# Kernel optimization log

Measured on AMD Instinct MI355X. Metric: run time of the kernel, lower is better.

Reference implementation:

```python
import jax, jax.numpy as jnp
import numpy as np

N = 10000        # nodes
E = 160000       # edges (before self-loops)
NFEAT = 256
NHID = 128
H = 4            # heads
NCLASS = 40
NLAYERS = 2
DT = 1.0
ALPHA = 1.0
GAMMA = 1.0
NEG_SLOPE = 0.2  # GATConv leaky_relu slope


def setup_inputs() -> dict:
    key = jax.random.key(0)
    ks = jax.random.split(key, 12)

    def glorot(k, shape):
        fan_in, fan_out = shape[-1], shape[0]
        lim = (6.0 / (fan_in + fan_out)) ** 0.5
        return jax.random.uniform(k, shape, jnp.float32, -lim, lim)

    return {
        "x": jax.random.normal(ks[0], (N, NFEAT), jnp.float32),
        "edge_index": jax.random.randint(ks[1], (2, E), 0, N, jnp.int64),
        "enc_w": glorot(ks[2], (NHID, NFEAT)),
        "enc_b": jnp.zeros((NHID,), jnp.float32),
        "res_w": glorot(ks[3], (H * NHID, NHID)),
        "res_b": jnp.zeros((H * NHID,), jnp.float32),
        "gat_w": glorot(ks[4], (H * NHID, NHID)),
        "att_src": glorot(ks[5], (H, NHID)) * 0.1,
        "att_dst": glorot(ks[6], (H, NHID)) * 0.1,
        "gat_b": jnp.zeros((H * NHID,), jnp.float32),
        "dec_w": glorot(ks[7], (NCLASS, NHID)),
        "dec_b": jnp.zeros((NCLASS,), jnp.float32),
    }


def _gat_conv(x, src, dst, gat_w, att_src, att_dst, gat_b):
    # x: [N, NHID] -> per-head features [N, H, C]
    xh = (x @ gat_w.T).reshape(N, H, NHID)
    a_src = jnp.sum(xh * att_src[None], axis=-1)  # [N, H]
    a_dst = jnp.sum(xh * att_dst[None], axis=-1)  # [N, H]
    e = jax.nn.leaky_relu(a_src[src] + a_dst[dst], NEG_SLOPE)  # [E', H]
    # segment softmax over incoming edges of each destination node
    m = jax.ops.segment_max(e, dst, num_segments=N)            # [N, H]
    e = jnp.exp(e - m[dst])
    s = jax.ops.segment_sum(e, dst, num_segments=N)            # [N, H]
    alpha = e / s[dst]                                          # [E', H]
    msg = xh[src] * alpha[:, :, None]                           # [E', H, C]
    out = jax.ops.segment_sum(msg, dst, num_segments=N)         # [N, H, C]
    return out.reshape(N, H * NHID) + gat_b


def reference(x, edge_index, enc_w, enc_b, res_w, res_b, gat_w,
              att_src, att_dst, gat_b, dec_w, dec_b):
    # add self-loops (GATConv default)
    loop = jnp.arange(N, dtype=edge_index.dtype)
    src = jnp.concatenate([edge_index[0], loop])
    dst = jnp.concatenate([edge_index[1], loop])

    Y = jax.nn.relu(x @ enc_w.T + enc_b)  # [N, NHID]
    X = Y
    for _ in range(NLAYERS):
        conv = _gat_conv(X, src, dst, gat_w, att_src, att_dst, gat_b)  # [N, H*NHID]
        res = X @ res_w.T + res_b                                       # [N, H*NHID]
        # faithful to .view(n_nodes, -1, nheads).mean(-1): [N, NHID, H] -> mean over heads axis
        z = jax.nn.elu(conv + res).reshape(N, NHID, H).mean(axis=-1)    # [N, NHID]
        Y = Y + DT * (z - ALPHA * Y - GAMMA * X)
        X = X + DT * Y
    return X @ dec_w.T + dec_b  # [N, NCLASS]
```

## Files before the change

kernel.cpp:

```cpp
#include <hip/hip_runtime.h>
#include <math.h>

#define NN 10000
#define EE 160000
#define EP 170000
#define NFEAT 256
#define NHID 128
#define NH 4
#define HF 512
#define NCLASS 40
#define FCOLS 1088

typedef __attribute__((ext_vector_type(8))) short bf8;
typedef __attribute__((ext_vector_type(8))) unsigned short u16x8;
typedef __attribute__((ext_vector_type(4))) float f4;

__device__ __forceinline__ float leaky02(float x) { return x >= 0.0f ? x : 0.2f * x; }

__device__ __forceinline__ unsigned short f2bf(float f) {
    unsigned u = __builtin_bit_cast(unsigned, f);
    unsigned r = (u + 0x7FFF + ((u >> 16) & 1)) >> 16;
    return (unsigned short)r;
}
__device__ __forceinline__ float bf2f(unsigned short h) {
    return __builtin_bit_cast(float, (unsigned)h << 16);
}

__device__ __forceinline__ int swz(int row, int c) {
    return ((((c >> 3) ^ (row & 7)) << 3) | (c & 7));
}

__device__ __forceinline__ void gl_lds16(const unsigned short* g, unsigned short* l)
{
    __builtin_amdgcn_global_load_lds(
        (const __attribute__((address_space(1))) unsigned int*)g,
        (__attribute__((address_space(3))) unsigned int*)l, 16, 0, 0);
}

#define C_X   2560000
#define C_EW  (C_X + 32768)
#define C_FW  (C_EW + 131072)
#define C_DW  (C_FW + 5120)
#define CVT_B  1333
#define ATTW_B (CVT_B + 8)
#define TOT_B  (ATTW_B + 166)

__global__ __launch_bounds__(256)
void fused0_k(const float* __restrict__ x, const float* __restrict__ enc_w,
              const float* __restrict__ gat_w, const float* __restrict__ res_w,
              const float* __restrict__ dec_w,
              const float* __restrict__ att_src, const float* __restrict__ att_dst,
              const float* __restrict__ res_b, const float* __restrict__ gat_b,
              const int* __restrict__ ei,
              unsigned short* __restrict__ xhi, unsigned short* __restrict__ ewhi,
              unsigned short* __restrict__ fwhi, unsigned short* __restrict__ dwhi,
              float* __restrict__ biasRG, int* __restrict__ cnt)
{
    int bId = blockIdx.x;
    int t = threadIdx.x;
    if (bId < CVT_B) {
        int iu = bId * 256 + t;
        int i = iu * 8;
        if (i >= C_DW) return;
        const float* src = nullptr; unsigned short* ph; int j, row, c, Kd;
        if (i < C_X)       { j = i;        src = x;     ph = xhi;
                             row = j >> 8; c = j & 255; Kd = 256; }
        else if (i < C_EW) { j = i - C_X;  src = enc_w; ph = ewhi;
                             row = j >> 8; c = j & 255; Kd = 256; }
        else if (i < C_FW) { j = i - C_EW; ph = fwhi;
                             row = j >> 7; c = j & 127; Kd = 128; }
        else               { j = i - C_FW; src = dec_w; ph = dwhi;
                             row = j >> 7; c = j & 127; Kd = 128; }
        float4 v0, v1;
        if (src) { v0 = *(const float4*)(src + j); v1 = *(const float4*)(src + j + 4); }
        else {
            const float* s2 = (j < 65536) ? (gat_w + j) : (res_w + j - 65536);
            v0 = *(const float4*)s2; v1 = *(const float4*)(s2 + 4);
        }
        float vv[8] = {v0.x, v0.y, v0.z, v0.w, v1.x, v1.y, v1.z, v1.w};
        unsigned short hs[8];
#pragma unroll
        for (int k = 0; k < 8; ++k) hs[k] = f2bf(vv[k]);
        int outp = row * Kd + swz(row, c);
        *(u16x8*)(ph + outp) = *(u16x8*)hs;
    } else if (bId < ATTW_B) {
        __shared__ float sm[256];
        int b = bId - CVT_B;
        int is_dst = b >> 2, h = b & 3;
        const float* att = is_dst ? att_dst : att_src;
        int k = t & 127, half = t >> 7;
        float s = 0.0f;
#pragma unroll 4
        for (int c = half * 64; c < half * 64 + 64; ++c)
            s = fmaf(gat_w[(size_t)(h * 128 + c) * 128 + k], att[h * 128 + c], s);
        sm[t] = s;
        __syncthreads();
        if (t < 128) {
            float v = sm[t] + sm[t + 128];
            int R = 1024 + is_dst * 4 + h;
            fwhi[(size_t)R * 128 + swz(R, k)] = f2bf(v);
        }
        for (int i = b * 896 + t; i < (b + 1) * 896; i += 256)
            fwhi[1032 * 128 + i] = 0;
        if (b < 2) {
            int c = b * 256 + t;
            biasRG[c] = res_b[c] + gat_b[c];
        }
    } else {
        for (int e = (bId - ATTW_B) * 256 + t; e < EP; e += (TOT_B - ATTW_B) * 256) {
            int d = (e < EE) ? ei[EE + e] : (e - EE);
            atomicAdd(&cnt[d], 1);
        }
    }
}

template<int MODE, int KTILES, int MERGE>
__global__ __launch_bounds__(256)
void gemm3_k(const unsigned short* __restrict__ A, const unsigned short* __restrict__ B,
             const float* __restrict__ bias, float* __restrict__ outF,
             unsigned short* __restrict__ outH, unsigned short* __restrict__ outL,
             float* __restrict__ a_src, float* __restrict__ a_dst, int M,
             const int* __restrict__ ei, const int* __restrict__ cnt,
             int* __restrict__ row_ptr, int* __restrict__ cursor, int* __restrict__ csr)
{
    constexpr int K = KTILES * 128;
    __shared__ __align__(16) unsigned short smem[2 * 64 * 128];
    const int tid = threadIdx.x;

    if (MERGE && blockIdx.y == gridDim.y - 1) {
        if (MERGE == 1) {
            if (blockIdx.x != 0) return;
            int* smi = (int*)smem;
            int i0 = tid * 40, i1 = min(i0 + 40, NN);
            int part = 0;
            for (int i = i0; i < i1; ++i) part += cnt[i];
            smi[tid] = part;
            __syncthreads();
            for (int off = 1; off < 256; off <<= 1) {
                int v = (tid >= off) ? smi[tid - off] : 0;
                __syncthreads();
                smi[tid] += v;
                __syncthreads();
            }
            int run = smi[tid] - part;
            for (int i = i0; i < i1; ++i) { row_ptr[i] = run; run += cnt[i]; }
            if (tid == 255) row_ptr[NN] = run;
        } else {
            int stride = gridDim.x * 256;
            for (int e = blockIdx.x * 256 + tid; e < EP; e += stride) {
                int s, d;
                if (e < EE) { s = ei[e]; d = ei[EE + e]; } else { s = e - EE; d = s; }
                int pos = row_ptr[d] + atomicAdd(&cursor[d], 1);
                csr[pos] = s;
            }
        }
        return;
    }

    unsigned short* sA = smem;
    unsigned short* sB = smem + 8192;

    const int lane = tid & 63, wv = tid >> 6;
    const int wr = (wv >> 1) * 32, wc = (wv & 1) * 32;
    const int bm = blockIdx.x * 64, bn = blockIdx.y * 64;
    const int r16 = lane & 15, q4 = lane >> 4;

    f4 acc[2][2];
#pragma unroll
    for (int i = 0; i < 2; ++i)
#pragma unroll
        for (int j = 0; j < 2; ++j) acc[i][j] = (f4){0.f, 0.f, 0.f, 0.f};

    const int ra0 = wr + r16;
    const int rb0 = wc + r16;

    for (int kt = 0; kt < KTILES; ++kt) {
        if (kt) __syncthreads();
#pragma unroll
        for (int j = 0; j < 4; ++j) {
            int i = tid + j * 256;
            int row = i >> 4, u = i & 15;
            int arow = min(bm + row, M - 1);
            size_t ga = (size_t)arow * K + kt * 128 + u * 8;
            size_t gb = (size_t)(bn + row) * K + kt * 128 + u * 8;
            int lb = (wv * 64 + j * 256) * 8;
            gl_lds16(A + ga, sA + lb);
            gl_lds16(B + gb, sB + lb);
        }
        __syncthreads();

#pragma unroll
        for (int ks = 0; ks < 4; ++ks) {
            int u = ks * 4 + q4;
            int oa0 = ra0 * 128 + ((u ^ (ra0 & 7)) * 8);
            int ob0 = rb0 * 128 + ((u ^ (rb0 & 7)) * 8);
            int oa1 = oa0 + 16 * 128;
            int ob1 = ob0 + 16 * 128;
            bf8 A0 = *(const bf8*)(sA + oa0);
            bf8 A1 = *(const bf8*)(sA + oa1);
            bf8 B0 = *(const bf8*)(sB + ob0);
            bf8 B1 = *(const bf8*)(sB + ob1);

            acc[0][0] = __builtin_amdgcn_mfma_f32_16x16x32_bf16(A0, B0, acc[0][0], 0, 0, 0);
            acc[0][1] = __builtin_amdgcn_mfma_f32_16x16x32_bf16(A0, B1, acc[0][1], 0, 0, 0);
            acc[1][0] = __builtin_amdgcn_mfma_f32_16x16x32_bf16(A1, B0, acc[1][0], 0, 0, 0);
            acc[1][1] = __builtin_amdgcn_mfma_f32_16x16x32_bf16(A1, B1, acc[1][1], 0, 0, 0);
        }
    }

    const int rbase = q4 * 4;

    if (MODE == 0 || (MODE == 2 && bn >= 1024)) {
#pragma unroll
        for (int i = 0; i < 2; ++i)
#pragma unroll
            for (int j = 0; j < 2; ++j)
#pragma unroll
                for (int r = 0; r < 4; ++r) {
                    int row = bm + wr + i * 16 + rbase + r;
                    int col = bn + wc + j * 16 + r16;
                    if (row >= M) continue;
                    float v = acc[i][j][r];
                    if (MODE == 0) {
                        if (col < NCLASS)
                            outF[(size_t)row * NCLASS + col] = v + bias[col];
                    } else {
                        if (col < 1032) {
                            int h = col - 1024;
                            if (h < 4) a_src[row * 4 + h] = v;
                            else       a_dst[row * 4 + h - 4] = v;
                        }
                    }
                }
        return;
    }

    __syncthreads();
    float* sC = (float*)smem;
#pragma unroll
    for (int i = 0; i < 2; ++i)
#pragma unroll
        for (int j = 0; j < 2; ++j)
#pragma unroll
            for (int r = 0; r < 4; ++r)
                sC[(wr + i * 16 + rbase + r) * 65 + (wc + j * 16 + r16)] = acc[i][j][r];
    __syncthreads();

    int row = tid >> 2, seg = tid & 3, c0 = seg * 16;
    int grow = bm + row;
    if (grow < M) {
        float v[16];
#pragma unroll
        for (int k = 0; k < 16; ++k) v[k] = sC[row * 65 + c0 + k];

        if (MODE == 1) {
            unsigned short hs[16];
#pragma unroll
            for (int k = 0; k < 16; ++k)
                hs[k] = f2bf(fmaxf(v[k] + bias[bn + c0 + k], 0.0f));
#pragma unroll
            for (int uu = 0; uu < 2; ++uu) {
                int ug = (bn + c0) / 8 + uu;
                int pu = ug ^ (grow & 7);
                *(u16x8*)(outH + (size_t)grow * 128 + pu * 8) = *(u16x8*)(hs + uu * 8);
            }
        } else {
            if (bn < 512) {
                unsigned short hs[16];
#pragma unroll
                for (int k = 0; k < 16; ++k) hs[k] = f2bf(v[k]);
                *(u16x8*)(outH + (size_t)grow * 512 + bn + c0)     = *(u16x8*)hs;
                *(u16x8*)(outH + (size_t)grow * 512 + bn + c0 + 8) = *(u16x8*)(hs + 8);
            } else {
                unsigned short hs[16];
#pragma unroll
                for (int k = 0; k < 16; ++k) hs[k] = f2bf(v[k] + bias[bn - 512 + c0 + k]);
                *(u16x8*)(outL + (size_t)grow * 512 + (bn - 512) + c0)     = *(u16x8*)hs;
                *(u16x8*)(outL + (size_t)grow * 512 + (bn - 512) + c0 + 8) = *(u16x8*)(hs + 8);
            }
        }
    }
}

__global__ __launch_bounds__(256)
void agg_k(const int* __restrict__ row_ptr, const int* __restrict__ csr,
           const float* __restrict__ a_src, const float* __restrict__ a_dst,
           const unsigned short* __restrict__ xh_b, const unsigned short* __restrict__ resb,
           unsigned short* __restrict__ Xhi)
{
    int bx = blockIdx.x;
    int h  = bx / 2500;
    int ng = bx - h * 2500;
    int wv = threadIdx.x >> 6, lane = threadIdx.x & 63;
    int d = ng * 4 + wv;
    int beg = row_ptr[d], end = row_ptr[d + 1];
    int eg = lane >> 4, c16 = lane & 15;
    int cb = h * 128 + c16 * 8;
    float ad = a_dst[d * 4 + h];
    u16x8 rv = *(const u16x8*)(resb + (size_t)d * HF + cb);

    float acc[8];
#pragma unroll
    for (int k = 0; k < 8; ++k) acc[k] = 0.0f;
    float ssum = 0.0f;

    int e = beg;
    for (; e + 16 <= end; e += 16) {
        int sv[4]; float w[4]; u16x8 v[4];
#pragma unroll
        for (int q = 0; q < 4; ++q) sv[q] = csr[e + q * 4 + eg];
#pragma unroll
        for (int q = 0; q < 4; ++q) v[q] = *(const u16x8*)(xh_b + (size_t)sv[q] * HF + cb);
#pragma unroll
        for (int q = 0; q < 4; ++q) {
            w[q] = __expf(leaky02(a_src[sv[q] * 4 + h] + ad));
            ssum += w[q];
        }
#pragma unroll
        for (int q = 0; q < 4; ++q)
#pragma unroll
            for (int k = 0; k < 8; ++k) acc[k] = fmaf(w[q], bf2f(v[q][k]), acc[k]);
    }
    for (; e + 4 <= end; e += 4) {
        int s = csr[e + eg];
        u16x8 v = *(const u16x8*)(xh_b + (size_t)s * HF + cb);
        float w = __expf(leaky02(a_src[s * 4 + h] + ad));
        ssum += w;
#pragma unroll
        for (int k = 0; k < 8; ++k) acc[k] = fmaf(w, bf2f(v[k]), acc[k]);
    }
    if (e + eg < end) {
        int s = csr[e + eg];
        u16x8 v = *(const u16x8*)(xh_b + (size_t)s * HF + cb);
        float w = __expf(leaky02(a_src[s * 4 + h] + ad));
        ssum += w;
#pragma unroll
        for (int k = 0; k < 8; ++k) acc[k] = fmaf(w, bf2f(v[k]), acc[k]);
    }

#pragma unroll
    for (int off = 16; off <= 32; off <<= 1) {
        ssum += __shfl_xor(ssum, off);
#pragma unroll
        for (int k = 0; k < 8; ++k) acc[k] += __shfl_xor(acc[k], off);
    }

    float inv = 1.0f / ssum;
    float uv[8];
#pragma unroll
    for (int k = 0; k < 8; ++k) {
        float v = fmaf(acc[k], inv, bf2f(rv[k]));
        uv[k] = (v > 0.0f) ? v : expm1f(v);
    }
    float z0 = (uv[0] + uv[1] + uv[2] + uv[3]) * 0.25f;
    float z1 = (uv[4] + uv[5] + uv[6] + uv[7]) * 0.25f;
    if (eg == 0) {
        int col = h * 32 + c16 * 2;
        unsigned short h0b = f2bf(z0), h1b = f2bf(z1);
        size_t idx = (size_t)d * NHID + swz(d, col);
        *(unsigned*)(Xhi + idx) = ((unsigned)h1b << 16) | h0b;
    }
}

extern "C" void kernel_launch(void* const* d_in, const int* in_sizes, int n_in,
                              void* d_out, int out_size, void* d_ws, size_t ws_size,
                              hipStream_t stream)
{
    const float* x       = (const float*)d_in[0];
    const int*   ei      = (const int*)d_in[1];
    const float* enc_w   = (const float*)d_in[2];
    const float* enc_b   = (const float*)d_in[3];
    const float* res_w   = (const float*)d_in[4];
    const float* res_b   = (const float*)d_in[5];
    const float* gat_w   = (const float*)d_in[6];
    const float* att_src = (const float*)d_in[7];
    const float* att_dst = (const float*)d_in[8];
    const float* gat_b   = (const float*)d_in[9];
    const float* dec_w   = (const float*)d_in[10];
    const float* dec_b   = (const float*)d_in[11];
    float* out = (float*)d_out;

    char* p = (char*)d_ws;
    auto alloc = [&](size_t bytes) -> void* {
        void* r = (void*)p;
        p += (bytes + 255) & ~(size_t)255;
        return r;
    };
    float* a_src  = (float*)alloc(40000 * 4);
    float* a_dst  = (float*)alloc(40000 * 4);
    float* biasRG = (float*)alloc(512 * 4);
    unsigned short* xh_b = (unsigned short*)alloc(5120000 * 2);
    unsigned short* resb = (unsigned short*)alloc(5120000 * 2);
    unsigned short* Xhi  = (unsigned short*)alloc(1280000 * 2);
    unsigned short* xhi  = (unsigned short*)alloc(2560000 * 2);
    unsigned short* ewhi = (unsigned short*)alloc(32768 * 2);
    unsigned short* fwhi = (unsigned short*)alloc(FCOLS * 128 * 2);
    int* row_ptr = (int*)alloc(10004 * 4);
    int* csr     = (int*)alloc(170000 * 4);
    char* zbase = p;
    unsigned short* dwhi = (unsigned short*)alloc(8192 * 2);
    int* cnt    = (int*)alloc(10000 * 4);
    int* cursor = (int*)alloc(10000 * 4);
    size_t zbytes = (size_t)(p - zbase);

    hipMemsetAsync(zbase, 0, zbytes, stream);

    fused0_k<<<TOT_B, 256, 0, stream>>>(
        x, enc_w, gat_w, res_w, dec_w, att_src, att_dst, res_b, gat_b, ei,
        xhi, ewhi, fwhi, dwhi, biasRG, cnt);

    gemm3_k<1, 2, 1><<<dim3(157, 3), 256, 0, stream>>>(
        xhi, ewhi, enc_b, nullptr, Xhi, nullptr, nullptr, nullptr, NN,
        nullptr, cnt, row_ptr, nullptr, nullptr);

    gemm3_k<2, 1, 2><<<dim3(157, 18), 256, 0, stream>>>(
        Xhi, fwhi, biasRG, nullptr, xh_b, resb, a_src, a_dst, NN,
        ei, nullptr, row_ptr, cursor, csr);
    agg_k<<<10000, 256, 0, stream>>>(row_ptr, csr, a_src, a_dst, xh_b, resb, Xhi);

    gemm3_k<2, 1, 0><<<dim3(157, 17), 256, 0, stream>>>(
        Xhi, fwhi, biasRG, nullptr, xh_b, resb, a_src, a_dst, NN,
        nullptr, nullptr, nullptr, nullptr, nullptr);
    agg_k<<<10000, 256, 0, stream>>>(row_ptr, csr, a_src, a_dst, xh_b, resb, Xhi);

    gemm3_k<0, 1, 0><<<dim3(157, 1), 256, 0, stream>>>(
        Xhi, dwhi, dec_b, out, nullptr, nullptr, nullptr, nullptr, NN,
        nullptr, nullptr, nullptr, nullptr, nullptr);
}
```

Measured before the change: 206.8 us.

## Merge all stages into one persistent cooperative kernel with grid syncs

```diff
diff --git a/kernel.cpp b/kernel.cpp
--- a/kernel.cpp
+++ b/kernel.cpp
@@ -1,5 +1,8 @@
 #include <hip/hip_runtime.h>
+#include <hip/hip_cooperative_groups.h>
 #include <math.h>
+
+namespace cg = cooperative_groups;
 
 #define NN 10000
 #define EE 160000
@@ -9,7 +12,6 @@
 #define NH 4
 #define HF 512
 #define NCLASS 40
-#define FCOLS 1088
 
 typedef __attribute__((ext_vector_type(8))) short bf8;
 typedef __attribute__((ext_vector_type(8))) unsigned short u16x8;
@@ -41,129 +43,27 @@
 #define C_EW  (C_X + 32768)
 #define C_FW  (C_EW + 131072)
 #define C_DW  (C_FW + 5120)
-#define CVT_B  1333
-#define ATTW_B (CVT_B + 8)
-#define TOT_B  (ATTW_B + 166)
-
-__global__ __launch_bounds__(256)
-void fused0_k(const float* __restrict__ x, const float* __restrict__ enc_w,
-              const float* __restrict__ gat_w, const float* __restrict__ res_w,
-              const float* __restrict__ dec_w,
-              const float* __restrict__ att_src, const float* __restrict__ att_dst,
-              const float* __restrict__ res_b, const float* __restrict__ gat_b,
-              const int* __restrict__ ei,
-              unsigned short* __restrict__ xhi, unsigned short* __restrict__ ewhi,
-              unsigned short* __restrict__ fwhi, unsigned short* __restrict__ dwhi,
-              float* __restrict__ biasRG, int* __restrict__ cnt)
-{
-    int bId = blockIdx.x;
-    int t = threadIdx.x;
-    if (bId < CVT_B) {
-        int iu = bId * 256 + t;
-        int i = iu * 8;
-        if (i >= C_DW) return;
-        const float* src = nullptr; unsigned short* ph; int j, row, c, Kd;
-        if (i < C_X)       { j = i;        src = x;     ph = xhi;
-                             row = j >> 8; c = j & 255; Kd = 256; }
-        else if (i < C_EW) { j = i - C_X;  src = enc_w; ph = ewhi;
-                             row = j >> 8; c = j & 255; Kd = 256; }
-        else if (i < C_FW) { j = i - C_EW; ph = fwhi;
-                             row = j >> 7; c = j & 127; Kd = 128; }
-        else               { j = i - C_FW; src = dec_w; ph = dwhi;
-                             row = j >> 7; c = j & 127; Kd = 128; }
-        float4 v0, v1;
-        if (src) { v0 = *(const float4*)(src + j); v1 = *(const float4*)(src + j + 4); }
-        else {
-            const float* s2 = (j < 65536) ? (gat_w + j) : (res_w + j - 65536);
-            v0 = *(const float4*)s2; v1 = *(const float4*)(s2 + 4);
-        }
-        float vv[8] = {v0.x, v0.y, v0.z, v0.w, v1.x, v1.y, v1.z, v1.w};
-        unsigned short hs[8];
-#pragma unroll
-        for (int k = 0; k < 8; ++k) hs[k] = f2bf(vv[k]);
-        int outp = row * Kd + swz(row, c);
-        *(u16x8*)(ph + outp) = *(u16x8*)hs;
-    } else if (bId < ATTW_B) {
-        __shared__ float sm[256];
-        int b = bId - CVT_B;
-        int is_dst = b >> 2, h = b & 3;
-        const float* att = is_dst ? att_dst : att_src;
-        int k = t & 127, half = t >> 7;
-        float s = 0.0f;
-#pragma unroll 4
-        for (int c = half * 64; c < half * 64 + 64; ++c)
-            s = fmaf(gat_w[(size_t)(h * 128 + c) * 128 + k], att[h * 128 + c], s);
-        sm[t] = s;
-        __syncthreads();
-        if (t < 128) {
-            float v = sm[t] + sm[t + 128];
-            int R = 1024 + is_dst * 4 + h;
-            fwhi[(size_t)R * 128 + swz(R, k)] = f2bf(v);
-        }
-        for (int i = b * 896 + t; i < (b + 1) * 896; i += 256)
-            fwhi[1032 * 128 + i] = 0;
-        if (b < 2) {
-            int c = b * 256 + t;
-            biasRG[c] = res_b[c] + gat_b[c];
-        }
-    } else {
-        for (int e = (bId - ATTW_B) * 256 + t; e < EP; e += (TOT_B - ATTW_B) * 256) {
-            int d = (e < EE) ? ei[EE + e] : (e - EE);
-            atomicAdd(&cnt[d], 1);
-        }
-    }
-}
-
-template<int MODE, int KTILES, int MERGE>
-__global__ __launch_bounds__(256)
-void gemm3_k(const unsigned short* __restrict__ A, const unsigned short* __restrict__ B,
-             const float* __restrict__ bias, float* __restrict__ outF,
-             unsigned short* __restrict__ outH, unsigned short* __restrict__ outL,
-             float* __restrict__ a_src, float* __restrict__ a_dst, int M,
-             const int* __restrict__ ei, const int* __restrict__ cnt,
-             int* __restrict__ row_ptr, int* __restrict__ cursor, int* __restrict__ csr)
+#define CVT_U (C_DW / 8)
+
+template<int MODE, int KTILES>
+__device__ void gemm_job(int bx, int by,
+    const unsigned short* __restrict__ A, const unsigned short* __restrict__ B,
+    const float* __restrict__ bias, float* __restrict__ outF,
+    unsigned short* __restrict__ outH, unsigned short* __restrict__ outL,
+    float* __restrict__ a_srcW, float* __restrict__ a_dstW, int M,
+    unsigned short* smem)
 {
     constexpr int K = KTILES * 128;
-    __shared__ __align__(16) unsigned short smem[2 * 64 * 128];
     const int tid = threadIdx.x;
-
-    if (MERGE && blockIdx.y == gridDim.y - 1) {
-        if (MERGE == 1) {
-            if (blockIdx.x != 0) return;
-            int* smi = (int*)smem;
-            int i0 = tid * 40, i1 = min(i0 + 40, NN);
-            int part = 0;
-            for (int i = i0; i < i1; ++i) part += cnt[i];
-            smi[tid] = part;
-            __syncthreads();
-            for (int off = 1; off < 256; off <<= 1) {
-                int v = (tid >= off) ? smi[tid - off] : 0;
-                __syncthreads();
-                smi[tid] += v;
-                __syncthreads();
-            }
-            int run = smi[tid] - part;
-            for (int i = i0; i < i1; ++i) { row_ptr[i] = run; run += cnt[i]; }
-            if (tid == 255) row_ptr[NN] = run;
-        } else {
-            int stride = gridDim.x * 256;
-            for (int e = blockIdx.x * 256 + tid; e < EP; e += stride) {
-                int s, d;
-                if (e < EE) { s = ei[e]; d = ei[EE + e]; } else { s = e - EE; d = s; }
-                int pos = row_ptr[d] + atomicAdd(&cursor[d], 1);
-                csr[pos] = s;
-            }
-        }
-        return;
-    }
-
     unsigned short* sA = smem;
     unsigned short* sB = smem + 8192;
 
     const int lane = tid & 63, wv = tid >> 6;
     const int wr = (wv >> 1) * 32, wc = (wv & 1) * 32;
-    const int bm = blockIdx.x * 64, bn = blockIdx.y * 64;
+    const int bm = bx * 64, bn = by * 64;
     const int r16 = lane & 15, q4 = lane >> 4;
+
+    __syncthreads();
 
     f4 acc[2][2];
 #pragma unroll
@@ -227,8 +127,8 @@
                     } else {
                         if (col < 1032) {
                             int h = col - 1024;
-                            if (h < 4) a_src[row * 4 + h] = v;
-                            else       a_dst[row * 4 + h - 4] = v;
+                            if (h < 4) a_srcW[row * 4 + h] = v;
+                            else       a_dstW[row * 4 + h - 4] = v;
                         }
                     }
                 }
@@ -282,13 +182,12 @@
     }
 }
 
-__global__ __launch_bounds__(256)
-void agg_k(const int* __restrict__ row_ptr, const int* __restrict__ csr,
-           const float* __restrict__ a_src, const float* __restrict__ a_dst,
-           const unsigned short* __restrict__ xh_b, const unsigned short* __restrict__ resb,
-           unsigned short* __restrict__ Xhi)
+__device__ void agg_job(int bx,
+    const int* __restrict__ row_ptr, const int* __restrict__ csr,
+    const float* __restrict__ a_src, const float* __restrict__ a_dst,
+    const unsigned short* __restrict__ xh_b, const unsigned short* __restrict__ resb,
+    unsigned short* __restrict__ Xhi)
 {
-    int bx = blockIdx.x;
     int h  = bx / 2500;
     int ng = bx - h * 2500;
     int wv = threadIdx.x >> 6, lane = threadIdx.x & 63;
@@ -362,23 +261,181 @@
     }
 }
 
+struct MegaArgs {
+    const float *x, *enc_w, *enc_b, *res_b, *gat_w, *att_src, *att_dst, *gat_b, *dec_w, *dec_b;
+    const float *res_w;
+    const int* ei;
+    float* out;
+    float *a_src, *a_dst, *biasRG;
+    unsigned short *xh_b, *resb, *Xhi, *xhi, *ewhi, *fwhi, *dwhi;
+    int *row_ptr, *csr, *cnt, *cursor;
+};
+
+__global__ __launch_bounds__(256, 3)
+void mega_k(MegaArgs a)
+{
+    __shared__ __align__(16) unsigned short smem[2 * 64 * 128];
+    cg::grid_group gg = cg::this_grid();
+    const int g   = (int)gridDim.x;
+    const int bid = (int)blockIdx.x, tid = (int)threadIdx.x;
+    const int gtid = bid * 256 + tid;
+    const int gth  = g * 256;
+
+    {
+        int* dz = (int*)(a.dwhi + 40 * 128);
+        for (int i = gtid; i < 1536; i += gth) dz[i] = 0;
+        for (int i = gtid; i < NN; i += gth) { a.cnt[i] = 0; a.cursor[i] = 0; }
+    }
+    for (int iu = gtid; iu < CVT_U; iu += gth) {
+        int i = iu * 8;
+        const float* src = nullptr; unsigned short* ph; int j, row, c, Kd;
+        if (i < C_X)       { j = i;        src = a.x;     ph = a.xhi;
+                             row = j >> 8; c = j & 255; Kd = 256; }
+        else if (i < C_EW) { j = i - C_X;  src = a.enc_w; ph = a.ewhi;
+                             row = j >> 8; c = j & 255; Kd = 256; }
+        else if (i < C_FW) { j = i - C_EW; ph = a.fwhi;
+                             row = j >> 7; c = j & 127; Kd = 128; }
+        else               { j = i - C_FW; src = a.dec_w; ph = a.dwhi;
+                             row = j >> 7; c = j & 127; Kd = 128; }
+        float4 v0, v1;
+        if (src) { v0 = *(const float4*)(src + j); v1 = *(const float4*)(src + j + 4); }
+        else {
+            const float* s2 = (j < 65536) ? (a.gat_w + j) : (a.res_w + j - 65536);
+            v0 = *(const float4*)s2; v1 = *(const float4*)(s2 + 4);
+        }
+        float vv[8] = {v0.x, v0.y, v0.z, v0.w, v1.x, v1.y, v1.z, v1.w};
+        unsigned short hs[8];
+#pragma unroll
+        for (int k = 0; k < 8; ++k) hs[k] = f2bf(vv[k]);
+        int outp = row * Kd + swz(row, c);
+        *(u16x8*)(ph + outp) = *(u16x8*)hs;
+    }
+    if (bid < 8) {
+        float* sm = (float*)smem;
+        int b = bid, is_dst = b >> 2, h = b & 3;
+        const float* att = is_dst ? a.att_dst : a.att_src;
+        int k = tid & 127, half = tid >> 7;
+        float s = 0.0f;
+#pragma unroll 4
+        for (int c = half * 64; c < half * 64 + 64; ++c)
+            s = fmaf(a.gat_w[(size_t)(h * 128 + c) * 128 + k], att[h * 128 + c], s);
+        sm[tid] = s;
+        __syncthreads();
+        if (tid < 128) {
+            float v = sm[tid] + sm[tid + 128];
+            int R = 1024 + is_dst * 4 + h;
+            a.fwhi[(size_t)R * 128 + swz(R, k)] = f2bf(v);
+        }
+        for (int i = b * 896 + tid; i < (b + 1) * 896; i += 256)
+            a.fwhi[1032 * 128 + i] = 0;
+    }
+    if (bid == 8) {
+        a.biasRG[tid]       = a.res_b[tid]       + a.gat_b[tid];
+        a.biasRG[tid + 256] = a.res_b[tid + 256] + a.gat_b[tid + 256];
+    }
+    gg.sync();
+
+    {
+        int gb1 = min(314, g - 128);
+        if (bid < gb1) {
+            for (int j = bid; j < 314; j += gb1)
+                gemm_job<1, 2>(j % 157, j / 157, a.xhi, a.ewhi, a.enc_b,
+                               nullptr, a.Xhi, nullptr, nullptr, nullptr, NN, smem);
+        } else {
+            for (int e = (bid - gb1) * 256 + tid; e < EP; e += (g - gb1) * 256) {
+                int d = (e < EE) ? a.ei[EE + e] : (e - EE);
+                atomicAdd(&a.cnt[d], 1);
+            }
+        }
+    }
+    gg.sync();
+
+    {
+        int gb2 = g - 1;
+        if (bid < gb2) {
+            int cpb = (2669 + gb2 - 1) / gb2;
+            int j0 = bid * cpb, j1 = min(j0 + cpb, 2669);
+            for (int j = j0; j < j1; ++j)
+                gemm_job<2, 1>(j % 157, j / 157, a.Xhi, a.fwhi, a.biasRG,
+                               nullptr, a.xh_b, a.resb, a.a_src, a.a_dst, NN, smem);
+        } else {
+            int* smi = (int*)smem;
+            int i0 = tid * 40, i1 = min(i0 + 40, NN);
+            int part = 0;
+            for (int i = i0; i < i1; ++i) part += a.cnt[i];
+            smi[tid] = part;
+            __syncthreads();
+            for (int off = 1; off < 256; off <<= 1) {
+                int v = (tid >= off) ? smi[tid - off] : 0;
+                __syncthreads();
+                smi[tid] += v;
+                __syncthreads();
+            }
+            int run = smi[tid] - part;
+            for (int i = i0; i < i1; ++i) { a.row_ptr[i] = run; run += a.cnt[i]; }
+            if (tid == 255) a.row_ptr[NN] = run;
+        }
+    }
+    gg.sync();
+
+    for (int e = gtid; e < EP; e += gth) {
+        int s, d;
+        if (e < EE) { s = a.ei[e]; d = a.ei[EE + e]; } else { s = e - EE; d = s; }
+        int pos = a.row_ptr[d] + atomicAdd(&a.cursor[d], 1);
+        a.csr[pos] = s;
+    }
+    gg.sync();
+
+    {
+        int cpb = (NN + g - 1) / g;
+        int j0 = bid * cpb, j1 = min(j0 + cpb, NN);
+        for (int j = j0; j < j1; ++j)
+            agg_job(j, a.row_ptr, a.csr, a.a_src, a.a_dst, a.xh_b, a.resb, a.Xhi);
+    }
+    gg.sync();
+
+    {
+        int cpb = (2669 + g - 1) / g;
+        int j0 = bid * cpb, j1 = min(j0 + cpb, 2669);
+        for (int j = j0; j < j1; ++j)
+            gemm_job<2, 1>(j % 157, j / 157, a.Xhi, a.fwhi, a.biasRG,
+                           nullptr, a.xh_b, a.resb, a.a_src, a.a_dst, NN, smem);
+    }
+    gg.sync();
+
+    {
+        int cpb = (NN + g - 1) / g;
+        int j0 = bid * cpb, j1 = min(j0 + cpb, NN);
+        for (int j = j0; j < j1; ++j)
+            agg_job(j, a.row_ptr, a.csr, a.a_src, a.a_dst, a.xh_b, a.resb, a.Xhi);
+    }
+    gg.sync();
+
+    if (bid < 157)
+        gemm_job<0, 1>(bid, 0, a.Xhi, a.dwhi, a.dec_b, a.out,
+                       nullptr, nullptr, nullptr, nullptr, NN, smem);
+}
+
 extern "C" void kernel_launch(void* const* d_in, const int* in_sizes, int n_in,
                               void* d_out, int out_size, void* d_ws, size_t ws_size,
                               hipStream_t stream)
 {
-    const float* x       = (const float*)d_in[0];
-    const int*   ei      = (const int*)d_in[1];
-    const float* enc_w   = (const float*)d_in[2];
-    const float* enc_b   = (const float*)d_in[3];
-    const float* res_w   = (const float*)d_in[4];
-    const float* res_b   = (const float*)d_in[5];
-    const float* gat_w   = (const float*)d_in[6];
-    const float* att_src = (const float*)d_in[7];
-    const float* att_dst = (const float*)d_in[8];
-    const float* gat_b   = (const float*)d_in[9];
-    const float* dec_w   = (const float*)d_in[10];
-    const float* dec_b   = (const float*)d_in[11];
-    float* out = (float*)d_out;
+    (void)in_sizes; (void)n_in; (void)out_size; (void)ws_size;
+
+    MegaArgs a;
+    a.x       = (const float*)d_in[0];
+    a.ei      = (const int*)d_in[1];
+    a.enc_w   = (const float*)d_in[2];
+    a.enc_b   = (const float*)d_in[3];
+    a.res_w   = (const float*)d_in[4];
+    a.res_b   = (const float*)d_in[5];
+    a.gat_w   = (const float*)d_in[6];
+    a.att_src = (const float*)d_in[7];
+    a.att_dst = (const float*)d_in[8];
+    a.gat_b   = (const float*)d_in[9];
+    a.dec_w   = (const float*)d_in[10];
+    a.dec_b   = (const float*)d_in[11];
+    a.out     = (float*)d_out;
 
     char* p = (char*)d_ws;
     auto alloc = [&](size_t bytes) -> void* {
@@ -386,44 +443,38 @@
         p += (bytes + 255) & ~(size_t)255;
         return r;
     };
-    float* a_src  = (float*)alloc(40000 * 4);
-    float* a_dst  = (float*)alloc(40000 * 4);
-    float* biasRG = (float*)alloc(512 * 4);
-    unsigned short* xh_b = (unsigned short*)alloc(5120000 * 2);
-    unsigned short* resb = (unsigned short*)alloc(5120000 * 2);
-    unsigned short* Xhi  = (unsigned short*)alloc(1280000 * 2);
-    unsigned short* xhi  = (unsigned short*)alloc(2560000 * 2);
-    unsigned short* ewhi = (unsigned short*)alloc(32768 * 2);
-    unsigned short* fwhi = (unsigned short*)alloc(FCOLS * 128 * 2);
-    int* row_ptr = (int*)alloc(10004 * 4);
-    int* csr     = (int*)alloc(170000 * 4);
-    char* zbase = p;
-    unsigned short* dwhi = (unsigned short*)alloc(8192 * 2);
-    int* cnt    = (int*)alloc(10000 * 4);
-    int* cursor = (int*)alloc(10000 * 4);
-    size_t zbytes = (size_t)(p - zbase);
-
-    hipMemsetAsync(zbase, 0, zbytes, stream);
-
-    fused0_k<<<TOT_B, 256, 0, stream>>>(
-        x, enc_w, gat_w, res_w, dec_w, att_src, att_dst, res_b, gat_b, ei,
-        xhi, ewhi, fwhi, dwhi, biasRG, cnt);
-
-    gemm3_k<1, 2, 1><<<dim3(157, 3), 256, 0, stream>>>(
-        xhi, ewhi, enc_b, nullptr, Xhi, nullptr, nullptr, nullptr, NN,
-        nullptr, cnt, row_ptr, nullptr, nullptr);
-
-    gemm3_k<2, 1, 2><<<dim3(157, 18), 256, 0, stream>>>(
-        Xhi, fwhi, biasRG, nullptr, xh_b, resb, a_src, a_dst, NN,
-        ei, nullptr, row_ptr, cursor, csr);
-    agg_k<<<10000, 256, 0, stream>>>(row_ptr, csr, a_src, a_dst, xh_b, resb, Xhi);
-
-    gemm3_k<2, 1, 0><<<dim3(157, 17), 256, 0, stream>>>(
-        Xhi, fwhi, biasRG, nullptr, xh_b, resb, a_src, a_dst, NN,
-        nullptr, nullptr, nullptr, nullptr, nullptr);
-    agg_k<<<10000, 256, 0, stream>>>(row_ptr, csr, a_src, a_dst, xh_b, resb, Xhi);
-
-    gemm3_k<0, 1, 0><<<dim3(157, 1), 256, 0, stream>>>(
-        Xhi, dwhi, dec_b, out, nullptr, nullptr, nullptr, nullptr, NN,
-        nullptr, nullptr, nullptr, nullptr, nullptr);
-}
+    a.a_src   = (float*)alloc(40000 * 4);
+    a.a_dst   = (float*)alloc(40000 * 4);
+    a.biasRG  = (float*)alloc(512 * 4);
+    a.xh_b    = (unsigned short*)alloc(5120000 * 2);
+    a.resb    = (unsigned short*)alloc(5120000 * 2);
+    a.Xhi     = (unsigned short*)alloc(1280000 * 2);
+    a.xhi     = (unsigned short*)alloc(2560000 * 2);
+    a.ewhi    = (unsigned short*)alloc(32768 * 2);
+    a.fwhi    = (unsigned short*)alloc(1088 * 128 * 2);
+    a.row_ptr = (int*)alloc(10004 * 4);
+    a.csr     = (int*)alloc(170000 * 4);
+    a.dwhi    = (unsigned short*)alloc(8192 * 2);
+    a.cnt     = (int*)alloc(10000 * 4);
+    a.cursor  = (int*)alloc(10000 * 4);
+
+    static int s_mb = 0;
+    if (s_mb == 0) {
+        int mb = 0;
+        if (hipOccupancyMaxActiveBlocksPerMultiprocessor(
+                &mb, (const void*)mega_k, 256, 0) != hipSuccess || mb < 1)
+            mb = 3;
+        if (mb > 5) mb = 5;
+        if (mb < 2) mb = 2;
+        s_mb = mb;
+    }
+    void* kargs[] = { (void*)&a };
+    for (int t = 0; t < 3; ++t) {
+        hipError_t err = hipLaunchCooperativeKernel(
+            (const void*)mega_k, dim3(256u * (unsigned)s_mb), dim3(256),
+            kargs, 0, stream);
+        if (err == hipSuccess) break;
+        (void)hipGetLastError();
+        if (s_mb > 1) --s_mb;
+    }
+}
```

After: 754.7 us. 3.65x slower.

## Convert x/enc_w to bf16 inside encoder GEMM and fuse attention logits into epilogue

Applied to the files above, without the earlier changes.

```diff
diff --git a/kernel.cpp b/kernel.cpp
--- a/kernel.cpp
+++ b/kernel.cpp
@@ -9,7 +9,6 @@
 #define NH 4
 #define HF 512
 #define NCLASS 40
-#define FCOLS 1088
 
 typedef __attribute__((ext_vector_type(8))) short bf8;
 typedef __attribute__((ext_vector_type(8))) unsigned short u16x8;
@@ -37,89 +36,52 @@
         (__attribute__((address_space(3))) unsigned int*)l, 16, 0, 0);
 }
 
-#define C_X   2560000
-#define C_EW  (C_X + 32768)
-#define C_FW  (C_EW + 131072)
-#define C_DW  (C_FW + 5120)
-#define CVT_B  1333
-#define ATTW_B (CVT_B + 8)
-#define TOT_B  (ATTW_B + 166)
+#define CVT_EL 136192
+#define CVT_B  67
+#define TOT_B  188
 
 __global__ __launch_bounds__(256)
-void fused0_k(const float* __restrict__ x, const float* __restrict__ enc_w,
-              const float* __restrict__ gat_w, const float* __restrict__ res_w,
+void fused0_k(const float* __restrict__ gat_w, const float* __restrict__ res_w,
               const float* __restrict__ dec_w,
-              const float* __restrict__ att_src, const float* __restrict__ att_dst,
               const float* __restrict__ res_b, const float* __restrict__ gat_b,
               const int* __restrict__ ei,
-              unsigned short* __restrict__ xhi, unsigned short* __restrict__ ewhi,
               unsigned short* __restrict__ fwhi, unsigned short* __restrict__ dwhi,
               float* __restrict__ biasRG, int* __restrict__ cnt)
 {
-    int bId = blockIdx.x;
-    int t = threadIdx.x;
+    int bId = blockIdx.x, t = threadIdx.x;
     if (bId < CVT_B) {
         int iu = bId * 256 + t;
         int i = iu * 8;
-        if (i >= C_DW) return;
-        const float* src = nullptr; unsigned short* ph; int j, row, c, Kd;
-        if (i < C_X)       { j = i;        src = x;     ph = xhi;
-                             row = j >> 8; c = j & 255; Kd = 256; }
-        else if (i < C_EW) { j = i - C_X;  src = enc_w; ph = ewhi;
-                             row = j >> 8; c = j & 255; Kd = 256; }
-        else if (i < C_FW) { j = i - C_EW; ph = fwhi;
-                             row = j >> 7; c = j & 127; Kd = 128; }
-        else               { j = i - C_FW; src = dec_w; ph = dwhi;
-                             row = j >> 7; c = j & 127; Kd = 128; }
-        float4 v0, v1;
-        if (src) { v0 = *(const float4*)(src + j); v1 = *(const float4*)(src + j + 4); }
-        else {
-            const float* s2 = (j < 65536) ? (gat_w + j) : (res_w + j - 65536);
-            v0 = *(const float4*)s2; v1 = *(const float4*)(s2 + 4);
-        }
+        if (i >= CVT_EL) return;
+        const float* src; unsigned short* ph; int j;
+        if (i < 131072) { j = i;          ph = fwhi;
+                          src = (j < 65536) ? (gat_w + j) : (res_w + j - 65536); }
+        else            { j = i - 131072; ph = dwhi; src = dec_w + j; }
+        int row = j >> 7, c = j & 127;
+        float4 v0 = *(const float4*)src, v1 = *(const float4*)(src + 4);
         float vv[8] = {v0.x, v0.y, v0.z, v0.w, v1.x, v1.y, v1.z, v1.w};
         unsigned short hs[8];
 #pragma unroll
         for (int k = 0; k < 8; ++k) hs[k] = f2bf(vv[k]);
-        int outp = row * Kd + swz(row, c);
-        *(u16x8*)(ph + outp) = *(u16x8*)hs;
-    } else if (bId < ATTW_B) {
-        __shared__ float sm[256];
-        int b = bId - CVT_B;
-        int is_dst = b >> 2, h = b & 3;
-        const float* att = is_dst ? att_dst : att_src;
-        int k = t & 127, half = t >> 7;
-        float s = 0.0f;
-#pragma unroll 4
-        for (int c = half * 64; c < half * 64 + 64; ++c)
-            s = fmaf(gat_w[(size_t)(h * 128 + c) * 128 + k], att[h * 128 + c], s);
-        sm[t] = s;
-        __syncthreads();
-        if (t < 128) {
-            float v = sm[t] + sm[t + 128];
-            int R = 1024 + is_dst * 4 + h;
-            fwhi[(size_t)R * 128 + swz(R, k)] = f2bf(v);
-        }
-        for (int i = b * 896 + t; i < (b + 1) * 896; i += 256)
-            fwhi[1032 * 128 + i] = 0;
-        if (b < 2) {
-            int c = b * 256 + t;
-            biasRG[c] = res_b[c] + gat_b[c];
-        }
+        *(u16x8*)(ph + row * 128 + swz(row, c)) = *(u16x8*)hs;
+    } else if (bId == CVT_B) {
+        biasRG[t]       = res_b[t]       + gat_b[t];
+        biasRG[t + 256] = res_b[t + 256] + gat_b[t + 256];
     } else {
-        for (int e = (bId - ATTW_B) * 256 + t; e < EP; e += (TOT_B - ATTW_B) * 256) {
+        for (int e = (bId - CVT_B - 1) * 256 + t; e < EP; e += (TOT_B - CVT_B - 1) * 256) {
             int d = (e < EE) ? ei[EE + e] : (e - EE);
             atomicAdd(&cnt[d], 1);
         }
     }
 }
 
-template<int MODE, int KTILES, int MERGE>
+template<int MODE, int KTILES, int MERGE, bool F32>
 __global__ __launch_bounds__(256)
-void gemm3_k(const unsigned short* __restrict__ A, const unsigned short* __restrict__ B,
+void gemm3_k(const void* __restrict__ Ap, const void* __restrict__ Bp,
              const float* __restrict__ bias, float* __restrict__ outF,
              unsigned short* __restrict__ outH, unsigned short* __restrict__ outL,
-             float* __restrict__ a_src, float* __restrict__ a_dst, int M,
+             float* __restrict__ aS, float* __restrict__ aD,
+             const float* __restrict__ attS, const float* __restrict__ attD, int M,
              const int* __restrict__ ei, const int* __restrict__ cnt,
              int* __restrict__ row_ptr, int* __restrict__ cursor, int* __restrict__ csr)
 {
@@ -176,16 +138,41 @@
 
     for (int kt = 0; kt < KTILES; ++kt) {
         if (kt) __syncthreads();
-#pragma unroll
-        for (int j = 0; j < 4; ++j) {
-            int i = tid + j * 256;
-            int row = i >> 4, u = i & 15;
-            int arow = min(bm + row, M - 1);
-            size_t ga = (size_t)arow * K + kt * 128 + u * 8;
-            size_t gb = (size_t)(bn + row) * K + kt * 128 + u * 8;
-            int lb = (wv * 64 + j * 256) * 8;
-            gl_lds16(A + ga, sA + lb);
-            gl_lds16(B + gb, sB + lb);
+        if (!F32) {
+            const unsigned short* A = (const unsigned short*)Ap;
+            const unsigned short* B = (const unsigned short*)Bp;
+#pragma unroll
+            for (int j = 0; j < 4; ++j) {
+                int i = tid + j * 256;
+                int row = i >> 4, u = i & 15;
+                int arow = min(bm + row, M - 1);
+                size_t ga = (size_t)arow * K + kt * 128 + u * 8;
+                size_t gb = (size_t)(bn + row) * K + kt * 128 + u * 8;
+                int lb = (wv * 64 + j * 256) * 8;
+                gl_lds16(A + ga, sA + lb);
+                gl_lds16(B + gb, sB + lb);
+            }
+        } else {
+            const float* A = (const float*)Ap;
+            const float* B = (const float*)Bp;
+#pragma unroll
+            for (int j = 0; j < 4; ++j) {
+                int i = tid + j * 256;
+                int row = i >> 4, u = i & 15;
+                int arow = min(bm + row, M - 1);
+                const float* pa = A + (size_t)arow * K + kt * 128 + u * 8;
+                const float* pb = B + (size_t)(bn + row) * K + kt * 128 + u * 8;
+                float4 a0 = *(const float4*)pa, a1 = *(const float4*)(pa + 4);
+                float4 b0 = *(const float4*)pb, b1 = *(const float4*)(pb + 4);
+                float av[8] = {a0.x, a0.y, a0.z, a0.w, a1.x, a1.y, a1.z, a1.w};
+                float bv[8] = {b0.x, b0.y, b0.z, b0.w, b1.x, b1.y, b1.z, b1.w};
+                unsigned short ha[8], hb[8];
+#pragma unroll
+                for (int k = 0; k < 8; ++k) { ha[k] = f2bf(av[k]); hb[k] = f2bf(bv[k]); }
+                int off = row * 128 + ((u ^ (row & 7)) * 8);
+                *(u16x8*)(sA + off) = *(u16x8*)ha;
+                *(u16x8*)(sB + off) = *(u16x8*)hb;
+            }
         }
         __syncthreads();
 
@@ -210,7 +197,7 @@
 
     const int rbase = q4 * 4;
 
-    if (MODE == 0 || (MODE == 2 && bn >= 1024)) {
+    if (MODE == 0) {
 #pragma unroll
         for (int i = 0; i < 2; ++i)
 #pragma unroll
@@ -219,18 +206,8 @@
                 for (int r = 0; r < 4; ++r) {
                     int row = bm + wr + i * 16 + rbase + r;
                     int col = bn + wc + j * 16 + r16;
-                    if (row >= M) continue;
-                    float v = acc[i][j][r];
-                    if (MODE == 0) {
-                        if (col < NCLASS)
-                            outF[(size_t)row * NCLASS + col] = v + bias[col];
-                    } else {
-                        if (col < 1032) {
-                            int h = col - 1024;
-                            if (h < 4) a_src[row * 4 + h] = v;
-                            else       a_dst[row * 4 + h - 4] = v;
-                        }
-                    }
+                    if (row >= M || col >= NCLASS) continue;
+                    outF[(size_t)row * NCLASS + col] = acc[i][j][r] + bias[col];
                 }
         return;
     }
@@ -271,6 +248,19 @@
                 for (int k = 0; k < 16; ++k) hs[k] = f2bf(v[k]);
                 *(u16x8*)(outH + (size_t)grow * 512 + bn + c0)     = *(u16x8*)hs;
                 *(u16x8*)(outH + (size_t)grow * 512 + bn + c0 + 8) = *(u16x8*)(hs + 8);
+                float ps = 0.0f, pd = 0.0f;
+#pragma unroll
+                for (int k = 0; k < 16; ++k) {
+                    ps = fmaf(v[k], attS[bn + c0 + k], ps);
+                    pd = fmaf(v[k], attD[bn + c0 + k], pd);
+                }
+                ps += __shfl_xor(ps, 1); ps += __shfl_xor(ps, 2);
+                pd += __shfl_xor(pd, 1); pd += __shfl_xor(pd, 2);
+                if (seg == 0) {
+                    int h = bn >> 7;
+                    atomicAdd(&aS[grow * 4 + h], ps);
+                    atomicAdd(&aD[grow * 4 + h], pd);
+                }
             } else {
                 unsigned short hs[16];
 #pragma unroll
@@ -386,44 +376,43 @@
         p += (bytes + 255) & ~(size_t)255;
         return r;
     };
-    float* a_src  = (float*)alloc(40000 * 4);
-    float* a_dst  = (float*)alloc(40000 * 4);
     float* biasRG = (float*)alloc(512 * 4);
     unsigned short* xh_b = (unsigned short*)alloc(5120000 * 2);
     unsigned short* resb = (unsigned short*)alloc(5120000 * 2);
     unsigned short* Xhi  = (unsigned short*)alloc(1280000 * 2);
-    unsigned short* xhi  = (unsigned short*)alloc(2560000 * 2);
-    unsigned short* ewhi = (unsigned short*)alloc(32768 * 2);
-    unsigned short* fwhi = (unsigned short*)alloc(FCOLS * 128 * 2);
+    unsigned short* fwhi = (unsigned short*)alloc(1024 * 128 * 2);
     int* row_ptr = (int*)alloc(10004 * 4);
     int* csr     = (int*)alloc(170000 * 4);
     char* zbase = p;
     unsigned short* dwhi = (unsigned short*)alloc(8192 * 2);
     int* cnt    = (int*)alloc(10000 * 4);
     int* cursor = (int*)alloc(10000 * 4);
+    float* aS1  = (float*)alloc(40000 * 4);
+    float* aD1  = (float*)alloc(40000 * 4);
+    float* aS2  = (float*)alloc(40000 * 4);
+    float* aD2  = (float*)alloc(40000 * 4);
     size_t zbytes = (size_t)(p - zbase);
 
     hipMemsetAsync(zbase, 0, zbytes, stream);
 
     fused0_k<<<TOT_B, 256, 0, stream>>>(
-        x, enc_w, gat_w, res_w, dec_w, att_src, att_dst, res_b, gat_b, ei,
-        xhi, ewhi, fwhi, dwhi, biasRG, cnt);
-
-    gemm3_k<1, 2, 1><<<dim3(157, 3), 256, 0, stream>>>(
-        xhi, ewhi, enc_b, nullptr, Xhi, nullptr, nullptr, nullptr, NN,
+        gat_w, res_w, dec_w, res_b, gat_b, ei, fwhi, dwhi, biasRG, cnt);
+
+    gemm3_k<1, 2, 1, true><<<dim3(157, 3), 256, 0, stream>>>(
+        x, enc_w, enc_b, nullptr, Xhi, nullptr, nullptr, nullptr, nullptr, nullptr, NN,
         nullptr, cnt, row_ptr, nullptr, nullptr);
 
-    gemm3_k<2, 1, 2><<<dim3(157, 18), 256, 0, stream>>>(
-        Xhi, fwhi, biasRG, nullptr, xh_b, resb, a_src, a_dst, NN,
+    gemm3_k<2, 1, 2, false><<<dim3(157, 17), 256, 0, stream>>>(
+        Xhi, fwhi, biasRG, nullptr, xh_b, resb, aS1, aD1, att_src, att_dst, NN,
         ei, nullptr, row_ptr, cursor, csr);
-    agg_k<<<10000, 256, 0, stream>>>(row_ptr, csr, a_src, a_dst, xh_b, resb, Xhi);
-
-    gemm3_k<2, 1, 0><<<dim3(157, 17), 256, 0, stream>>>(
-        Xhi, fwhi, biasRG, nullptr, xh_b, resb, a_src, a_dst, NN,
+    agg_k<<<10000, 256, 0, stream>>>(row_ptr, csr, aS1, aD1, xh_b, resb, Xhi);
+
+    gemm3_k<2, 1, 0, false><<<dim3(157, 16), 256, 0, stream>>>(
+        Xhi, fwhi, biasRG, nullptr, xh_b, resb, aS2, aD2, att_src, att_dst, NN,
         nullptr, nullptr, nullptr, nullptr, nullptr);
-    agg_k<<<10000, 256, 0, stream>>>(row_ptr, csr, a_src, a_dst, xh_b, resb, Xhi);
-
-    gemm3_k<0, 1, 0><<<dim3(157, 1), 256, 0, stream>>>(
-        Xhi, dwhi, dec_b, out, nullptr, nullptr, nullptr, nullptr, NN,
+    agg_k<<<10000, 256, 0, stream>>>(row_ptr, csr, aS2, aD2, xh_b, resb, Xhi);
+
+    gemm3_k<0, 1, 0, false><<<dim3(157, 1), 256, 0, stream>>>(
+        Xhi, dwhi, dec_b, out, nullptr, nullptr, nullptr, nullptr, nullptr, nullptr, NN,
         nullptr, nullptr, nullptr, nullptr, nullptr);
 }
```

Measured after the change: 206.5 us. No clear change (-0.1%).
